# Kernel tuning notes

Hardware: AMD Instinct MI355X
Metric: run time of the kernel (lower is better)

Reference implementation:

```python
import jax, jax.numpy as jnp
import numpy as np

N, E, DIN, DOUT = 30000, 480000, 512, 512


def setup_inputs() -> dict:
    key = jax.random.key(0)
    ks = jax.random.split(key, 20)
    inp = {}
    inp["x"] = jax.random.normal(ks[0], (N, DIN), jnp.float32)
    inp["edge_index"] = jax.random.randint(ks[1], (2, E), 0, N, dtype=jnp.int64)
    inp["edge_weight"] = jax.random.uniform(ks[2], (E,), jnp.float32)
    sc = 1.0 / np.sqrt(DIN)
    sl = 1.0 / np.sqrt(2 * DOUT)
    for i, g in enumerate(["i", "f", "g", "o"]):
        inp[f"Wc_{g}"] = jax.random.normal(ks[3 + 4 * i], (DIN, DOUT), jnp.float32) * sc
        inp[f"bc_{g}"] = jnp.zeros((DOUT,), jnp.float32)
        inp[f"Wl_{g}"] = jax.random.normal(ks[4 + 4 * i], (2 * DOUT, DOUT), jnp.float32) * sl
        inp[f"bl_{g}"] = jnp.zeros((DOUT,), jnp.float32)
    return inp


def _gcn_norm(src, dst, w, n):
    # add self loops with weight 1.0 (improved=False), then symmetric normalization
    loops = jnp.arange(n, dtype=src.dtype)
    src = jnp.concatenate([src, loops])
    dst = jnp.concatenate([dst, loops])
    w = jnp.concatenate([w, jnp.ones((n,), w.dtype)])
    deg = jax.ops.segment_sum(w, dst, num_segments=n)
    dinv = jnp.where(deg > 0, jax.lax.rsqrt(jnp.where(deg > 0, deg, 1.0)), 0.0)
    norm = dinv[src] * w * dinv[dst]
    return src, dst, norm


def reference(x, edge_index, edge_weight,
              Wc_i, bc_i, Wl_i, bl_i,
              Wc_f, bc_f, Wl_f, bl_f,
              Wc_g, bc_g, Wl_g, bl_g,
              Wc_o, bc_o, Wl_o, bl_o):
    n = x.shape[0]
    src, dst, norm = _gcn_norm(edge_index[0], edge_index[1], edge_weight, n)
    H = jnp.zeros((n, DOUT), x.dtype)  # _set_hidden_state default
    C = jnp.zeros((n, DOUT), x.dtype)  # _set_cell_state default

    def conv(Wc, bc):
        xw = x @ Wc                                        # [N, DOUT] dense GEMM
        agg = jax.ops.segment_sum(norm[:, None] * xw[src], dst, num_segments=n)
        return agg + bc

    def gate(Wc, bc, Wl, bl, act):
        z = jnp.concatenate([conv(Wc, bc), H], axis=1)      # [N, 2*DOUT]
        return act(z @ Wl + bl)

    I = gate(Wc_i, bc_i, Wl_i, bl_i, jax.nn.sigmoid)
    F = gate(Wc_f, bc_f, Wl_f, bl_f, jax.nn.sigmoid)
    G = gate(Wc_g, bc_g, Wl_g, bl_g, jnp.tanh)
    O = gate(Wc_o, bc_o, Wl_o, bl_o, jax.nn.sigmoid)
    Cn = F * C + I * G
    Hn = O * jnp.tanh(Cn)
    return O, Hn, Cn
```

## Files before the change

kernel.cpp:

```cpp
#include <hip/hip_runtime.h>
#include <stdint.h>

typedef __bf16 bf16;
typedef __attribute__((ext_vector_type(4))) float f4;
typedef __attribute__((ext_vector_type(4))) float f32x4;
typedef __attribute__((ext_vector_type(8))) __bf16 bf8v;
typedef __attribute__((ext_vector_type(4))) __bf16 bf4v;

#define NN 30000
#define MPAD 30080
#define OUTSTRIDE 15360000

typedef __attribute__((address_space(3))) unsigned int as3_u32;
typedef __attribute__((address_space(1))) unsigned int as1_u32;

__device__ __forceinline__ void gl_lds16(const void* g, void* l) {
  __builtin_amdgcn_global_load_lds((as1_u32*)g, (as3_u32*)l, 16, 0, 0);
}

__global__ void k_init(float* deg, int* counts, int* cursor, int n) {
  int i = blockIdx.x * 256 + threadIdx.x;
  if (i < n) { deg[i] = 1.0f; counts[i] = 0; cursor[i] = 0; }
}

__global__ void k_pre(const int* __restrict__ ei, const float* __restrict__ ew,
                      float* __restrict__ deg, int* __restrict__ counts, int E) {
  int e = blockIdx.x * 256 + threadIdx.x;
  if (e < E) {
    int d = ei[E + e];
    atomicAdd(&deg[d], ew[e]);
    atomicAdd(&counts[d], 1);
  }
}

__global__ void k_bsum(const int* __restrict__ counts, int* __restrict__ bsum,
                       float* __restrict__ dinv, int n) {
  __shared__ int sm[256];
  int i = blockIdx.x * 256 + threadIdx.x;
  sm[threadIdx.x] = (i < n) ? counts[i] : 0;
  if (i < n) { float d = dinv[i]; dinv[i] = d > 0.f ? rsqrtf(d) : 0.f; }
  __syncthreads();
  for (int st = 128; st > 0; st >>= 1) {
    if (threadIdx.x < st) sm[threadIdx.x] += sm[threadIdx.x + st];
    __syncthreads();
  }
  if (threadIdx.x == 0) bsum[blockIdx.x] = sm[0];
}

__global__ void k_bscan(int* bsum, int nb) {
  __shared__ int buf[128];
  int t = threadIdx.x;
  int v = (t < nb) ? bsum[t] : 0;
  buf[t] = v;
  __syncthreads();
  for (int s = 1; s < 128; s <<= 1) {
    int u = (t >= s) ? buf[t - s] : 0;
    __syncthreads();
    buf[t] += u;
    __syncthreads();
  }
  if (t < nb) bsum[t] = buf[t] - v;
}

__global__ void k_offs(const int* __restrict__ counts, const int* __restrict__ bsum,
                       int* __restrict__ offs, int n, int E) {
  __shared__ int buf[256];
  int i = blockIdx.x * 256 + threadIdx.x;
  int v = (i < n) ? counts[i] : 0;
  buf[threadIdx.x] = v;
  __syncthreads();
  for (int s = 1; s < 256; s <<= 1) {
    int u = (threadIdx.x >= s) ? buf[threadIdx.x - s] : 0;
    __syncthreads();
    buf[threadIdx.x] += u;
    __syncthreads();
  }
  if (i < n) offs[i] = bsum[blockIdx.x] + buf[threadIdx.x] - v;
  if (i == 0) offs[n] = E;
}

__global__ void k_scatter(const int* __restrict__ ei, const float* __restrict__ ew,
                          const float* __restrict__ dinv, const int* __restrict__ offs,
                          int* __restrict__ cursor, int* __restrict__ srcs,
                          float* __restrict__ norms, int E) {
  int e = blockIdx.x * 256 + threadIdx.x;
  if (e >= E) return;
  int s = ei[e], d = ei[E + e];
  int pos = offs[d] + atomicAdd(&cursor[d], 1);
  srcs[pos] = s;
  norms[pos] = dinv[s] * ew[e] * dinv[d];
}

__global__ void k_xbf(const float* __restrict__ x, bf16* __restrict__ xbf, int n8) {
  int i = blockIdx.x * 256 + threadIdx.x;
  if (i >= n8) return;
  const f4* x4 = (const f4*)x;
  f4 a = x4[2 * i], b = x4[2 * i + 1];
  bf8v o;
#pragma unroll
  for (int j = 0; j < 4; ++j) { o[j] = (bf16)a[j]; o[4 + j] = (bf16)b[j]; }
  ((bf8v*)xbf)[i] = o;
}

__global__ __launch_bounds__(256) void k_agg(const int* __restrict__ offs, const int* __restrict__ srcs,
                                             const float* __restrict__ norms,
                                             const float* __restrict__ dinv, const bf16* __restrict__ xbf,
                                             bf16* __restrict__ ybf) {
  int wv = (blockIdx.x * 256 + threadIdx.x) >> 6;
  int lane = threadIdx.x & 63;
  if (wv >= MPAD) return;
  bf16* yrow = ybf + ((size_t)wv << 9) + lane * 8;
  if (wv >= NN) {
    bf8v z;
#pragma unroll
    for (int j = 0; j < 8; ++j) z[j] = (bf16)0.f;
    *(bf8v*)yrow = z;
    return;
  }
  float acc[8];
  float s0 = dinv[wv]; s0 *= s0;
  bf8v xv0 = *(const bf8v*)(xbf + ((size_t)wv << 9) + lane * 8);
#pragma unroll
  for (int j = 0; j < 8; ++j) acc[j] = s0 * (float)xv0[j];
  int e = offs[wv], end = offs[wv + 1];
  for (; e + 2 <= end; e += 2) {
    int s1 = srcs[e], s2 = srcs[e + 1];
    float n1 = norms[e], n2 = norms[e + 1];
    bf8v v1 = *(const bf8v*)(xbf + ((size_t)s1 << 9) + lane * 8);
    bf8v v2 = *(const bf8v*)(xbf + ((size_t)s2 << 9) + lane * 8);
#pragma unroll
    for (int j = 0; j < 8; ++j) acc[j] += n1 * (float)v1[j] + n2 * (float)v2[j];
  }
  if (e < end) {
    int s1 = srcs[e]; float n1 = norms[e];
    bf8v v1 = *(const bf8v*)(xbf + ((size_t)s1 << 9) + lane * 8);
#pragma unroll
    for (int j = 0; j < 8; ++j) acc[j] += n1 * (float)v1[j];
  }
  bf8v o;
#pragma unroll
  for (int j = 0; j < 8; ++j) o[j] = (bf16)acc[j];
  *(bf8v*)yrow = o;
}

__global__ void k_wcomb(const float* __restrict__ WcA, const float* __restrict__ WlA,
                        const float* __restrict__ WcB, const float* __restrict__ WlB,
                        const float* __restrict__ WcC, const float* __restrict__ WlC,
                        bf16* __restrict__ Wt) {
  const float* Wc; const float* Wl;
  int g = blockIdx.z;
  if (g == 0)      { Wc = WcA; Wl = WlA; }
  else if (g == 1) { Wc = WcB; Wl = WlB; }
  else             { Wc = WcC; Wl = WlC; }
  int k0 = blockIdx.x * 64, j0 = blockIdx.y * 64;
  int t = threadIdx.x, tx = t & 15, ty = t >> 4;
  __shared__ float sWc[64][17];
  __shared__ float sWl[16][64];
  float acc[4][4] = {};
  for (int c0 = 0; c0 < 512; c0 += 16) {
    { int kk = t >> 2, c4 = (t & 3) * 4;
      f4 v = *(const f4*)(Wc + (size_t)(k0 + kk) * 512 + c0 + c4);
#pragma unroll
      for (int j = 0; j < 4; ++j) sWc[kk][c4 + j] = v[j]; }
    { int cc = t >> 4, j4 = (t & 15) * 4;
      f4 v = *(const f4*)(Wl + (size_t)(c0 + cc) * 512 + j0 + j4);
      *(f4*)&sWl[cc][j4] = v; }
    __syncthreads();
#pragma unroll
    for (int cc = 0; cc < 16; ++cc) {
      float wcv[4], wlv[4];
#pragma unroll
      for (int b = 0; b < 4; ++b) wcv[b] = sWc[tx * 4 + b][cc];
#pragma unroll
      for (int a = 0; a < 4; ++a) wlv[a] = sWl[cc][ty * 4 + a];
#pragma unroll
      for (int a = 0; a < 4; ++a)
#pragma unroll
        for (int b = 0; b < 4; ++b) acc[a][b] += wlv[a] * wcv[b];
    }
    __syncthreads();
  }
#pragma unroll
  for (int a = 0; a < 4; ++a) {
    bf4v o;
#pragma unroll
    for (int b = 0; b < 4; ++b) o[b] = (bf16)acc[a][b];
    *(bf4v*)&Wt[((size_t)g * 512 + j0 + ty * 4 + a) * 512 + k0 + tx * 4] = o;
  }
}

__global__ void k_bcomb3(const float* __restrict__ bcA, const float* __restrict__ blA, const float* __restrict__ WlA,
                         const float* __restrict__ bcB, const float* __restrict__ blB, const float* __restrict__ WlB,
                         const float* __restrict__ bcC, const float* __restrict__ blC, const float* __restrict__ WlC,
                         float* __restrict__ bcomb) {
  int g = blockIdx.x >> 3, jc = blockIdx.x & 7;
  const float* bc; const float* bl; const float* Wl;
  if (g == 0)      { bc = bcA; bl = blA; Wl = WlA; }
  else if (g == 1) { bc = bcB; bl = blB; Wl = WlB; }
  else             { bc = bcC; bl = blC; Wl = WlC; }
  int jl = threadIdx.x & 63, part = threadIdx.x >> 6;
  int j = jc * 64 + jl;
  float s = 0.f;
  for (int c = part * 128; c < part * 128 + 128; ++c)
    s += bc[c] * Wl[(size_t)c * 512 + j];
  __shared__ float sm[4][64];
  sm[part][jl] = s;
  __syncthreads();
  if (part == 0)
    bcomb[g * 512 + j] = bl[j] + sm[0][jl] + sm[1][jl] + sm[2][jl] + sm[3][jl];
}

__global__ __launch_bounds__(256, 3) void k_gemm(const bf16* __restrict__ A, const bf16* __restrict__ Bt,
                                                 const float* __restrict__ bcomb, float* __restrict__ out) {
  __shared__ __align__(16) char lds[40960];
  const int t = threadIdx.x, lane = t & 63, w = t >> 6;
  const int wm = w >> 1, wn = w & 1;
  const int d = blockIdx.x;
  const int s = (d & 7) * 235 + (d >> 3);
  const int m0 = (s >> 3) * 128, n0 = (s & 7) * 64;
  const int l15 = lane & 15, lhi = lane >> 4;
  f32x4 acc[3][4][2] = {};

  const int lq = lane >> 2;
  const int sw = (lane >> 3) & 3;
  const int kcol = 16 * ((lane & 3) ^ sw);
  const int rswz = 16 * (lhi ^ ((l15 >> 1) & 3));

  const char* aS[2];
#pragma unroll
  for (int i = 0; i < 2; ++i) {
    int r = (i * 4 + w) * 16 + lq;
    aS[i] = (const char*)A + ((size_t)(m0 + r) << 10) + kcol;
  }
  const char* bS[3];
#pragma unroll
  for (int i = 0; i < 3; ++i) {
    int bi = i * 4 + w, g = bi >> 2, q = bi & 3;
    int n = q * 16 + lq;
    bS[i] = (const char*)Bt + ((size_t)(g * 512 + n0 + n) << 10) + kcol;
  }
  const int vA = (wm * 64 + l15) * 64 + rswz;
  const int vB = 8192 + (wn * 32 + l15) * 64 + rswz;

  auto stage = [&](int bufoff, int kp) {
#pragma unroll
    for (int i = 0; i < 2; ++i)
      gl_lds16(aS[i] + kp * 64, lds + bufoff + (i * 4 + w) * 1024 + lane * 16);
#pragma unroll
    for (int i = 0; i < 3; ++i)
      gl_lds16(bS[i] + kp * 64, lds + bufoff + 8192 + (i * 4 + w) * 1024 + lane * 16);
  };

  auto compute = [&](int bufoff) {
    bf8v af[4];
#pragma unroll
    for (int mi = 0; mi < 4; ++mi)
      af[mi] = *(const bf8v*)(lds + bufoff + vA + mi * 1024);
#pragma unroll
    for (int g = 0; g < 3; ++g) {
      bf8v b0 = *(const bf8v*)(lds + bufoff + vB + g * 4096);
      bf8v b1 = *(const bf8v*)(lds + bufoff + vB + g * 4096 + 1024);
#pragma unroll
      for (int mi = 0; mi < 4; ++mi) {
        acc[g][mi][0] = __builtin_amdgcn_mfma_f32_16x16x32_bf16(b0, af[mi], acc[g][mi][0], 0, 0, 0);
        acc[g][mi][1] = __builtin_amdgcn_mfma_f32_16x16x32_bf16(b1, af[mi], acc[g][mi][1], 0, 0, 0);
      }
    }
  };

  stage(0, 0);
  stage(20480, 1);
#pragma unroll
  for (int kp = 0; kp < 16; ++kp) {
    if (kp < 15) asm volatile("s_waitcnt vmcnt(5)" ::: "memory");
    else         asm volatile("s_waitcnt vmcnt(0)" ::: "memory");
    __builtin_amdgcn_sched_barrier(0);
    __builtin_amdgcn_s_barrier();
    __builtin_amdgcn_sched_barrier(0);
    compute((kp & 1) * 20480);
    __builtin_amdgcn_sched_barrier(0);
    __builtin_amdgcn_s_barrier();
    __builtin_amdgcn_sched_barrier(0);
    if (kp < 14) stage((kp & 1) * 20480, kp + 2);
  }

#pragma unroll
  for (int ni = 0; ni < 2; ++ni) {
    int nb = n0 + wn * 32 + ni * 16 + lhi * 4;
    f4 bI = *(const f4*)&bcomb[nb];
    f4 bG = *(const f4*)&bcomb[512 + nb];
    f4 bO = *(const f4*)&bcomb[1024 + nb];
#pragma unroll
    for (int mi = 0; mi < 4; ++mi) {
      int row = m0 + wm * 64 + mi * 16 + l15;
      if (row < NN) {
        f4 vO, vH, vC;
#pragma unroll
        for (int r = 0; r < 4; ++r) {
          float zi = acc[0][mi][ni][r] + bI[r];
          float zg = acc[1][mi][ni][r] + bG[r];
          float zo = acc[2][mi][ni][r] + bO[r];
          float I = 1.f / (1.f + __expf(-zi));
          float e2g = __expf(2.f * zg);
          float G = (e2g - 1.f) / (e2g + 1.f);
          float O = 1.f / (1.f + __expf(-zo));
          float Cn = I * G;
          float e2c = __expf(2.f * Cn);
          float tc = (e2c - 1.f) / (e2c + 1.f);
          vO[r] = O; vH[r] = O * tc; vC[r] = Cn;
        }
        size_t base = ((size_t)row << 9) + nb;
        *(f4*)&out[base] = vO;
        *(f4*)&out[OUTSTRIDE + base] = vH;
        *(f4*)&out[2 * OUTSTRIDE + base] = vC;
      }
    }
  }
}

extern "C" void kernel_launch(void* const* d_in, const int* in_sizes, int n_in,
                              void* d_out, int out_size, void* d_ws, size_t ws_size,
                              hipStream_t stream) {
  const float* x   = (const float*)d_in[0];
  const int*   ei  = (const int*)d_in[1];
  const float* ew  = (const float*)d_in[2];
  const float* Wc_i = (const float*)d_in[3];
  const float* bc_i = (const float*)d_in[4];
  const float* Wl_i = (const float*)d_in[5];
  const float* bl_i = (const float*)d_in[6];
  const float* Wc_g = (const float*)d_in[11];
  const float* bc_g = (const float*)d_in[12];
  const float* Wl_g = (const float*)d_in[13];
  const float* bl_g = (const float*)d_in[14];
  const float* Wc_o = (const float*)d_in[15];
  const float* bc_o = (const float*)d_in[16];
  const float* Wl_o = (const float*)d_in[17];
  const float* bl_o = (const float*)d_in[18];

  const int E = in_sizes[2];
  const int n = in_sizes[0] / 512;
  const int NB = (n + 255) / 256;

  char* ws = (char*)d_ws;
  bf16*  ybf   = (bf16*)ws;
  float* dinv  = (float*)(ws + 30801920);
  bf16*  Wt    = (bf16*)(ws + 30924800);
  float* bcomb = (float*)(ws + 32497664);
  int*   bsum  = (int*)(ws + 32503808);
  (void)ws_size;

  char* ob = (char*)d_out;
  float* out   = (float*)d_out;
  bf16*  xbf   = (bf16*)ob;
  int*   srcs  = (int*)(ob + 30720000);
  float* norms = (float*)(ob + 32640000);
  int*   cnts  = (int*)(ob + 34560000);
  int*   offs  = (int*)(ob + 34680000);
  int*   curs  = (int*)(ob + 34800016);
  (void)out_size; (void)n_in;

  k_init<<<NB, 256, 0, stream>>>(dinv, cnts, curs, n);
  k_pre<<<(E + 255) / 256, 256, 0, stream>>>(ei, ew, dinv, cnts, E);
  k_bsum<<<NB, 256, 0, stream>>>(cnts, bsum, dinv, n);
  k_bscan<<<1, 128, 0, stream>>>(bsum, NB);
  k_offs<<<NB, 256, 0, stream>>>(cnts, bsum, offs, n, E);
  k_scatter<<<(E + 255) / 256, 256, 0, stream>>>(ei, ew, dinv, offs, curs, srcs, norms, E);
  k_xbf<<<(n * 512 / 8 + 255) / 256, 256, 0, stream>>>(x, xbf, n * 512 / 8);
  k_agg<<<(MPAD * 64 + 255) / 256, 256, 0, stream>>>(offs, srcs, norms, dinv, xbf, ybf);
  k_wcomb<<<dim3(8, 8, 3), 256, 0, stream>>>(Wc_i, Wl_i, Wc_g, Wl_g, Wc_o, Wl_o, Wt);
  k_bcomb3<<<24, 256, 0, stream>>>(bc_i, bl_i, Wl_i, bc_g, bl_g, Wl_g, bc_o, bl_o, Wl_o, bcomb);
  k_gemm<<<1880, 256, 0, stream>>>(ybf, Wt, bcomb, out);
}
```

Before: 308.9 us.

## Fuse edge scatter with weight/bias combine and pack src/norm pairs

The edge scatter, the weight-combine GEMM and the bias-combine kernels are merged into one launch, with each block picking its role by block index. Source index and norm are now stored as one int2 per edge, and degree and count are interleaved in a single array. The separate init kernel is replaced by one hipMemsetAsync that zeroes both that array and the cursors. The aggregation loop is unrolled to four edges so more gathers are in flight. The goal is fewer kernel launches and fewer scattered memory accesses in preprocessing and aggregation, at the cost of a larger branchy fused kernel and higher register pressure in the aggregation loop.

```diff
diff --git a/kernel.cpp b/kernel.cpp
--- a/kernel.cpp
+++ b/kernel.cpp
@@ -10,6 +10,7 @@
 #define NN 30000
 #define MPAD 30080
 #define OUTSTRIDE 15360000
+#define SC_B 1875
 
 typedef __attribute__((address_space(3))) unsigned int as3_u32;
 typedef __attribute__((address_space(1))) unsigned int as1_u32;
@@ -18,27 +19,27 @@
   __builtin_amdgcn_global_load_lds((as1_u32*)g, (as3_u32*)l, 16, 0, 0);
 }
 
-__global__ void k_init(float* deg, int* counts, int* cursor, int n) {
-  int i = blockIdx.x * 256 + threadIdx.x;
-  if (i < n) { deg[i] = 1.0f; counts[i] = 0; cursor[i] = 0; }
-}
-
 __global__ void k_pre(const int* __restrict__ ei, const float* __restrict__ ew,
-                      float* __restrict__ deg, int* __restrict__ counts, int E) {
+                      void* __restrict__ degcnt, int E) {
   int e = blockIdx.x * 256 + threadIdx.x;
   if (e < E) {
     int d = ei[E + e];
-    atomicAdd(&deg[d], ew[e]);
-    atomicAdd(&counts[d], 1);
-  }
-}
-
-__global__ void k_bsum(const int* __restrict__ counts, int* __restrict__ bsum,
+    atomicAdd((float*)degcnt + 2 * d, ew[e]);
+    atomicAdd((int*)degcnt + 2 * d + 1, 1);
+  }
+}
+
+__global__ void k_bsum(const void* __restrict__ degcnt, int* __restrict__ bsum,
                        float* __restrict__ dinv, int n) {
   __shared__ int sm[256];
   int i = blockIdx.x * 256 + threadIdx.x;
-  sm[threadIdx.x] = (i < n) ? counts[i] : 0;
-  if (i < n) { float d = dinv[i]; dinv[i] = d > 0.f ? rsqrtf(d) : 0.f; }
+  int cnt = 0;
+  if (i < n) {
+    int2 p = ((const int2*)degcnt)[i];
+    cnt = p.y;
+    dinv[i] = rsqrtf(__int_as_float(p.x) + 1.0f);
+  }
+  sm[threadIdx.x] = cnt;
   __syncthreads();
   for (int st = 128; st > 0; st >>= 1) {
     if (threadIdx.x < st) sm[threadIdx.x] += sm[threadIdx.x + st];
@@ -62,11 +63,11 @@
   if (t < nb) bsum[t] = buf[t] - v;
 }
 
-__global__ void k_offs(const int* __restrict__ counts, const int* __restrict__ bsum,
+__global__ void k_offs(const void* __restrict__ degcnt, const int* __restrict__ bsum,
                        int* __restrict__ offs, int n, int E) {
   __shared__ int buf[256];
   int i = blockIdx.x * 256 + threadIdx.x;
-  int v = (i < n) ? counts[i] : 0;
+  int v = (i < n) ? ((const int*)degcnt)[2 * i + 1] : 0;
   buf[threadIdx.x] = v;
   __syncthreads();
   for (int s = 1; s < 256; s <<= 1) {
@@ -77,18 +78,6 @@
   }
   if (i < n) offs[i] = bsum[blockIdx.x] + buf[threadIdx.x] - v;
   if (i == 0) offs[n] = E;
-}
-
-__global__ void k_scatter(const int* __restrict__ ei, const float* __restrict__ ew,
-                          const float* __restrict__ dinv, const int* __restrict__ offs,
-                          int* __restrict__ cursor, int* __restrict__ srcs,
-                          float* __restrict__ norms, int E) {
-  int e = blockIdx.x * 256 + threadIdx.x;
-  if (e >= E) return;
-  int s = ei[e], d = ei[E + e];
-  int pos = offs[d] + atomicAdd(&cursor[d], 1);
-  srcs[pos] = s;
-  norms[pos] = dinv[s] * ew[e] * dinv[d];
 }
 
 __global__ void k_xbf(const float* __restrict__ x, bf16* __restrict__ xbf, int n8) {
@@ -102,8 +91,87 @@
   ((bf8v*)xbf)[i] = o;
 }
 
-__global__ __launch_bounds__(256) void k_agg(const int* __restrict__ offs, const int* __restrict__ srcs,
-                                             const float* __restrict__ norms,
+__global__ void k_fused(const int* __restrict__ ei, const float* __restrict__ ew,
+                        const float* __restrict__ dinv, const int* __restrict__ offs,
+                        int* __restrict__ cursor, int2* __restrict__ sn, int E,
+                        const float* __restrict__ WcA, const float* __restrict__ WlA,
+                        const float* __restrict__ WcB, const float* __restrict__ WlB,
+                        const float* __restrict__ WcC, const float* __restrict__ WlC,
+                        bf16* __restrict__ Wt,
+                        const float* __restrict__ bcA, const float* __restrict__ blA,
+                        const float* __restrict__ bcB, const float* __restrict__ blB,
+                        const float* __restrict__ bcC, const float* __restrict__ blC,
+                        float* __restrict__ bcomb) {
+  __shared__ float sWc[64][17];
+  __shared__ float sWl[16][64];
+  __shared__ float smr[4][64];
+  int b = blockIdx.x;
+  if (b < SC_B) {
+    int e = b * 256 + threadIdx.x;
+    if (e >= E) return;
+    int s = ei[e], d = ei[E + e];
+    int pos = offs[d] + atomicAdd(&cursor[d], 1);
+    sn[pos] = make_int2(s, __float_as_int(dinv[s] * ew[e] * dinv[d]));
+  } else if (b < SC_B + 192) {
+    int bb = b - SC_B;
+    int g = bb >> 6, rem = bb & 63;
+    const float* Wc; const float* Wl;
+    if (g == 0)      { Wc = WcA; Wl = WlA; }
+    else if (g == 1) { Wc = WcB; Wl = WlB; }
+    else             { Wc = WcC; Wl = WlC; }
+    int k0 = (rem & 7) * 64, j0 = (rem >> 3) * 64;
+    int t = threadIdx.x, tx = t & 15, ty = t >> 4;
+    float acc[4][4] = {};
+    for (int c0 = 0; c0 < 512; c0 += 16) {
+      { int kk = t >> 2, c4 = (t & 3) * 4;
+        f4 v = *(const f4*)(Wc + (size_t)(k0 + kk) * 512 + c0 + c4);
+#pragma unroll
+        for (int j = 0; j < 4; ++j) sWc[kk][c4 + j] = v[j]; }
+      { int cc = t >> 4, j4 = (t & 15) * 4;
+        f4 v = *(const f4*)(Wl + (size_t)(c0 + cc) * 512 + j0 + j4);
+        *(f4*)&sWl[cc][j4] = v; }
+      __syncthreads();
+#pragma unroll
+      for (int cc = 0; cc < 16; ++cc) {
+        float wcv[4], wlv[4];
+#pragma unroll
+        for (int q = 0; q < 4; ++q) wcv[q] = sWc[tx * 4 + q][cc];
+#pragma unroll
+        for (int a = 0; a < 4; ++a) wlv[a] = sWl[cc][ty * 4 + a];
+#pragma unroll
+        for (int a = 0; a < 4; ++a)
+#pragma unroll
+          for (int q = 0; q < 4; ++q) acc[a][q] += wlv[a] * wcv[q];
+      }
+      __syncthreads();
+    }
+#pragma unroll
+    for (int a = 0; a < 4; ++a) {
+      bf4v o;
+#pragma unroll
+      for (int q = 0; q < 4; ++q) o[q] = (bf16)acc[a][q];
+      *(bf4v*)&Wt[((size_t)g * 512 + j0 + ty * 4 + a) * 512 + k0 + tx * 4] = o;
+    }
+  } else {
+    int bb = b - SC_B - 192;
+    int g = bb >> 3, jc = bb & 7;
+    const float* bc; const float* bl; const float* Wl;
+    if (g == 0)      { bc = bcA; bl = blA; Wl = WlA; }
+    else if (g == 1) { bc = bcB; bl = blB; Wl = WlB; }
+    else             { bc = bcC; bl = blC; Wl = WlC; }
+    int jl = threadIdx.x & 63, part = threadIdx.x >> 6;
+    int j = jc * 64 + jl;
+    float s = 0.f;
+    for (int c = part * 128; c < part * 128 + 128; ++c)
+      s += bc[c] * Wl[(size_t)c * 512 + j];
+    smr[part][jl] = s;
+    __syncthreads();
+    if (part == 0)
+      bcomb[g * 512 + j] = bl[j] + smr[0][jl] + smr[1][jl] + smr[2][jl] + smr[3][jl];
+  }
+}
+
+__global__ __launch_bounds__(256) void k_agg(const int* __restrict__ offs, const int2* __restrict__ sn,
                                              const float* __restrict__ dinv, const bf16* __restrict__ xbf,
                                              bf16* __restrict__ ybf) {
   int wv = (blockIdx.x * 256 + threadIdx.x) >> 6;
@@ -123,91 +191,29 @@
 #pragma unroll
   for (int j = 0; j < 8; ++j) acc[j] = s0 * (float)xv0[j];
   int e = offs[wv], end = offs[wv + 1];
-  for (; e + 2 <= end; e += 2) {
-    int s1 = srcs[e], s2 = srcs[e + 1];
-    float n1 = norms[e], n2 = norms[e + 1];
-    bf8v v1 = *(const bf8v*)(xbf + ((size_t)s1 << 9) + lane * 8);
-    bf8v v2 = *(const bf8v*)(xbf + ((size_t)s2 << 9) + lane * 8);
-#pragma unroll
-    for (int j = 0; j < 8; ++j) acc[j] += n1 * (float)v1[j] + n2 * (float)v2[j];
-  }
-  if (e < end) {
-    int s1 = srcs[e]; float n1 = norms[e];
-    bf8v v1 = *(const bf8v*)(xbf + ((size_t)s1 << 9) + lane * 8);
-#pragma unroll
-    for (int j = 0; j < 8; ++j) acc[j] += n1 * (float)v1[j];
+  for (; e + 4 <= end; e += 4) {
+    int2 p0 = sn[e], p1 = sn[e + 1], p2 = sn[e + 2], p3 = sn[e + 3];
+    bf8v v0 = *(const bf8v*)(xbf + ((size_t)p0.x << 9) + lane * 8);
+    bf8v v1 = *(const bf8v*)(xbf + ((size_t)p1.x << 9) + lane * 8);
+    bf8v v2 = *(const bf8v*)(xbf + ((size_t)p2.x << 9) + lane * 8);
+    bf8v v3 = *(const bf8v*)(xbf + ((size_t)p3.x << 9) + lane * 8);
+    float n0 = __int_as_float(p0.y), n1 = __int_as_float(p1.y);
+    float n2 = __int_as_float(p2.y), n3 = __int_as_float(p3.y);
+#pragma unroll
+    for (int j = 0; j < 8; ++j)
+      acc[j] += n0 * (float)v0[j] + n1 * (float)v1[j] + n2 * (float)v2[j] + n3 * (float)v3[j];
+  }
+  for (; e < end; ++e) {
+    int2 p = sn[e];
+    bf8v v = *(const bf8v*)(xbf + ((size_t)p.x << 9) + lane * 8);
+    float nn = __int_as_float(p.y);
+#pragma unroll
+    for (int j = 0; j < 8; ++j) acc[j] += nn * (float)v[j];
   }
   bf8v o;
 #pragma unroll
   for (int j = 0; j < 8; ++j) o[j] = (bf16)acc[j];
   *(bf8v*)yrow = o;
-}
-
-__global__ void k_wcomb(const float* __restrict__ WcA, const float* __restrict__ WlA,
-                        const float* __restrict__ WcB, const float* __restrict__ WlB,
-                        const float* __restrict__ WcC, const float* __restrict__ WlC,
-                        bf16* __restrict__ Wt) {
-  const float* Wc; const float* Wl;
-  int g = blockIdx.z;
-  if (g == 0)      { Wc = WcA; Wl = WlA; }
-  else if (g == 1) { Wc = WcB; Wl = WlB; }
-  else             { Wc = WcC; Wl = WlC; }
-  int k0 = blockIdx.x * 64, j0 = blockIdx.y * 64;
-  int t = threadIdx.x, tx = t & 15, ty = t >> 4;
-  __shared__ float sWc[64][17];
-  __shared__ float sWl[16][64];
-  float acc[4][4] = {};
-  for (int c0 = 0; c0 < 512; c0 += 16) {
-    { int kk = t >> 2, c4 = (t & 3) * 4;
-      f4 v = *(const f4*)(Wc + (size_t)(k0 + kk) * 512 + c0 + c4);
-#pragma unroll
-      for (int j = 0; j < 4; ++j) sWc[kk][c4 + j] = v[j]; }
-    { int cc = t >> 4, j4 = (t & 15) * 4;
-      f4 v = *(const f4*)(Wl + (size_t)(c0 + cc) * 512 + j0 + j4);
-      *(f4*)&sWl[cc][j4] = v; }
-    __syncthreads();
-#pragma unroll
-    for (int cc = 0; cc < 16; ++cc) {
-      float wcv[4], wlv[4];
-#pragma unroll
-      for (int b = 0; b < 4; ++b) wcv[b] = sWc[tx * 4 + b][cc];
-#pragma unroll
-      for (int a = 0; a < 4; ++a) wlv[a] = sWl[cc][ty * 4 + a];
-#pragma unroll
-      for (int a = 0; a < 4; ++a)
-#pragma unroll
-        for (int b = 0; b < 4; ++b) acc[a][b] += wlv[a] * wcv[b];
-    }
-    __syncthreads();
-  }
-#pragma unroll
-  for (int a = 0; a < 4; ++a) {
-    bf4v o;
-#pragma unroll
-    for (int b = 0; b < 4; ++b) o[b] = (bf16)acc[a][b];
-    *(bf4v*)&Wt[((size_t)g * 512 + j0 + ty * 4 + a) * 512 + k0 + tx * 4] = o;
-  }
-}
-
-__global__ void k_bcomb3(const float* __restrict__ bcA, const float* __restrict__ blA, const float* __restrict__ WlA,
-                         const float* __restrict__ bcB, const float* __restrict__ blB, const float* __restrict__ WlB,
-                         const float* __restrict__ bcC, const float* __restrict__ blC, const float* __restrict__ WlC,
-                         float* __restrict__ bcomb) {
-  int g = blockIdx.x >> 3, jc = blockIdx.x & 7;
-  const float* bc; const float* bl; const float* Wl;
-  if (g == 0)      { bc = bcA; bl = blA; Wl = WlA; }
-  else if (g == 1) { bc = bcB; bl = blB; Wl = WlB; }
-  else             { bc = bcC; bl = blC; Wl = WlC; }
-  int jl = threadIdx.x & 63, part = threadIdx.x >> 6;
-  int j = jc * 64 + jl;
-  float s = 0.f;
-  for (int c = part * 128; c < part * 128 + 128; ++c)
-    s += bc[c] * Wl[(size_t)c * 512 + j];
-  __shared__ float sm[4][64];
-  sm[part][jl] = s;
-  __syncthreads();
-  if (part == 0)
-    bcomb[g * 512 + j] = bl[j] + sm[0][jl] + sm[1][jl] + sm[2][jl] + sm[3][jl];
 }
 
 __global__ __launch_bounds__(256, 3) void k_gemm(const bf16* __restrict__ A, const bf16* __restrict__ Bt,
@@ -350,24 +356,23 @@
   (void)ws_size;
 
   char* ob = (char*)d_out;
-  float* out   = (float*)d_out;
-  bf16*  xbf   = (bf16*)ob;
-  int*   srcs  = (int*)(ob + 30720000);
-  float* norms = (float*)(ob + 32640000);
-  int*   cnts  = (int*)(ob + 34560000);
-  int*   offs  = (int*)(ob + 34680000);
-  int*   curs  = (int*)(ob + 34800016);
+  float* out    = (float*)d_out;
+  bf16*  xbf    = (bf16*)ob;
+  int2*  sn     = (int2*)(ob + 30720000);
+  void*  degcnt = (void*)(ob + 34560000);
+  int*   curs   = (int*)(ob + 34800000);
+  int*   offs   = (int*)(ob + 34920000);
   (void)out_size; (void)n_in;
 
-  k_init<<<NB, 256, 0, stream>>>(dinv, cnts, curs, n);
-  k_pre<<<(E + 255) / 256, 256, 0, stream>>>(ei, ew, dinv, cnts, E);
-  k_bsum<<<NB, 256, 0, stream>>>(cnts, bsum, dinv, n);
+  hipMemsetAsync(degcnt, 0, 360000, stream);
+  k_xbf<<<(n * 512 / 8 + 255) / 256, 256, 0, stream>>>(x, xbf, n * 512 / 8);
+  k_pre<<<(E + 255) / 256, 256, 0, stream>>>(ei, ew, degcnt, E);
+  k_bsum<<<NB, 256, 0, stream>>>(degcnt, bsum, dinv, n);
   k_bscan<<<1, 128, 0, stream>>>(bsum, NB);
-  k_offs<<<NB, 256, 0, stream>>>(cnts, bsum, offs, n, E);
-  k_scatter<<<(E + 255) / 256, 256, 0, stream>>>(ei, ew, dinv, offs, curs, srcs, norms, E);
-  k_xbf<<<(n * 512 / 8 + 255) / 256, 256, 0, stream>>>(x, xbf, n * 512 / 8);
-  k_agg<<<(MPAD * 64 + 255) / 256, 256, 0, stream>>>(offs, srcs, norms, dinv, xbf, ybf);
-  k_wcomb<<<dim3(8, 8, 3), 256, 0, stream>>>(Wc_i, Wl_i, Wc_g, Wl_g, Wc_o, Wl_o, Wt);
-  k_bcomb3<<<24, 256, 0, stream>>>(bc_i, bl_i, Wl_i, bc_g, bl_g, Wl_g, bc_o, bl_o, Wl_o, bcomb);
+  k_offs<<<NB, 256, 0, stream>>>(degcnt, bsum, offs, n, E);
+  k_fused<<<SC_B + 192 + 24, 256, 0, stream>>>(ei, ew, dinv, offs, curs, sn, E,
+                                               Wc_i, Wl_i, Wc_g, Wl_g, Wc_o, Wl_o, Wt,
+                                               bc_i, bl_i, bc_g, bl_g, bc_o, bl_o, bcomb);
+  k_agg<<<(MPAD * 64 + 255) / 256, 256, 0, stream>>>(offs, sn, dinv, xbf, ybf);
   k_gemm<<<1880, 256, 0, stream>>>(ybf, Wt, bcomb, out);
 }
```

After: 301.1 us. -2.5%, faster.
